# Kernel optimization log

Hardware: AMD Instinct MI355X
Metric: run time of the kernel (lower is better)

## Reference

```python
import jax, jax.numpy as jnp
import numpy as np

MODEL_DIM = 1024
NUM_HEADS = 16
K_DIM = MODEL_DIM // NUM_HEADS


def setup_inputs() -> dict:
    key = jax.random.key(0)
    k1, k2, k3 = jax.random.split(key, 3)
    x = jax.random.normal(k1, (4, 2048, MODEL_DIM), dtype=jnp.float32)
    # nn.Linear(model_dim, 3*model_dim, bias=False): store as [D, 3D] so y = x @ W
    wqkv = jax.random.normal(k2, (MODEL_DIM, 3 * MODEL_DIM), dtype=jnp.float32) * (MODEL_DIM ** -0.5)
    wo = jax.random.normal(k3, (MODEL_DIM, MODEL_DIM), dtype=jnp.float32) * (MODEL_DIM ** -0.5)
    return {"x": x, "wqkv": wqkv, "wo": wo}


def reference(x, wqkv, wo):
    B, L, D = x.shape
    H, K = NUM_HEADS, K_DIM
    qkv = jnp.einsum("bld,de->ble", x, wqkv)  # [B, L, 3D]
    q, k, v = jnp.split(qkv, 3, axis=-1)
    # Faithful to source: plain reshape (no transpose) into [B, H, L, K]
    qh = q.reshape(B, H, L, K)
    kh = k.reshape(B, H, L, K)
    vh = v.reshape(B, H, L, K)
    scores = jnp.einsum("bhlk,bhmk->bhlm", qh, kh) / jnp.sqrt(jnp.float32(K))
    # Faithful quirk: softmax over dim=1 (head axis), as in the source
    probs = jax.nn.softmax(scores, axis=1)
    attended = jnp.einsum("bhlm,bhmk->bhlk", probs, vh)  # [B, H, L, K]
    concatted = attended.transpose(0, 2, 1, 3).reshape(B, L, D)
    return jnp.einsum("bld,de->ble", concatted, wo)
```

## Files before the change

### kernel.cpp

```cpp
#include <hip/hip_runtime.h>
#include <hip/hip_bf16.h>
#include <stdint.h>

typedef __attribute__((ext_vector_type(8))) short short8;
typedef __attribute__((ext_vector_type(4))) float floatx4;

#define QSCALE 0.18033688f

__device__ __forceinline__ unsigned short f2bf(float f) {
    unsigned int u = __float_as_uint(f);
    u += 0x7fffu + ((u >> 16) & 1u);
    return (unsigned short)(u >> 16);
}
__device__ __forceinline__ unsigned int pack2bf(float a, float b) {
    __hip_bfloat162 h = __float22bfloat162_rn(make_float2(a, b));
    return *reinterpret_cast<unsigned int*>(&h);
}

__device__ __forceinline__ void async16(const void* g, void* l) {
    __builtin_amdgcn_global_load_lds(
        (const __attribute__((address_space(1))) unsigned int*)g,
        (__attribute__((address_space(3))) unsigned int*)l, 16, 0, 0);
}

__global__ __launch_bounds__(256) void cvt_bf16(const float* __restrict__ src,
                                                unsigned short* __restrict__ dst, int n8) {
    int i = blockIdx.x * 256 + threadIdx.x;
    if (i >= n8) return;
    const float4 a = ((const float4*)src)[2 * i];
    const float4 b = ((const float4*)src)[2 * i + 1];
    ushort4 lo, hi;
    lo.x = f2bf(a.x); lo.y = f2bf(a.y); lo.z = f2bf(a.z); lo.w = f2bf(a.w);
    hi.x = f2bf(b.x); hi.y = f2bf(b.y); hi.z = f2bf(b.z); hi.w = f2bf(b.w);
    ((ushort4*)dst)[2 * i] = lo;
    ((ushort4*)dst)[2 * i + 1] = hi;
}

__global__ __launch_bounds__(256) void tcvt(const float* __restrict__ src,
                                            unsigned short* __restrict__ dst, int R, int C) {
    __shared__ unsigned short t[64][72];
    const int tid = threadIdx.x;
    const int r0 = blockIdx.y * 64, c0 = blockIdx.x * 64;
    #pragma unroll
    for (int it = 0; it < 4; it++) {
        int idx = it * 256 + tid;
        int rr = idx >> 4, cc = (idx & 15) * 4;
        float4 v = *(const float4*)(src + (size_t)(r0 + rr) * C + c0 + cc);
        t[cc + 0][rr] = f2bf(v.x);
        t[cc + 1][rr] = f2bf(v.y);
        t[cc + 2][rr] = f2bf(v.z);
        t[cc + 3][rr] = f2bf(v.w);
    }
    __syncthreads();
    #pragma unroll
    for (int it = 0; it < 2; it++) {
        int idx = it * 256 + tid;
        int cc = idx >> 3, r8 = (idx & 7) * 8;
        short8 v = *(const short8*)&t[cc][r8];
        *(short8*)(dst + (size_t)(c0 + cc) * R + r0 + r8) = v;
    }
}

__global__ __launch_bounds__(256) void vtrans(const unsigned short* __restrict__ vb,
                                              unsigned short* __restrict__ vbt) {
    __shared__ unsigned short t[64][72];
    const int tid = threadIdx.x;
    const int bh = blockIdx.y, m0 = blockIdx.x * 64;
    const unsigned short* src = vb + ((size_t)bh * 2048 + m0) * 64;
    unsigned short* dst = vbt + ((size_t)bh << 17) + m0;
    union { short8 v; unsigned short u[8]; } tmp;
    #pragma unroll
    for (int it = 0; it < 2; it++) {
        int idx = it * 256 + tid;
        int m = idx >> 3, c8 = (idx & 7) * 8;
        tmp.v = *(const short8*)(src + (size_t)m * 64 + c8);
        #pragma unroll
        for (int j = 0; j < 8; j++) t[c8 + j][m] = tmp.u[j];
    }
    __syncthreads();
    #pragma unroll
    for (int it = 0; it < 2; it++) {
        int idx = it * 256 + tid;
        int k = idx >> 3, c8 = (idx & 7) * 8;
        short8 v = *(const short8*)&t[k][c8];
        *(short8*)(dst + (size_t)k * 2048 + c8) = v;
    }
}

__global__ __launch_bounds__(256) void qkv_gemm(
    const unsigned short* __restrict__ A, const unsigned short* __restrict__ Bt,
    unsigned short* __restrict__ qb, unsigned short* __restrict__ kb,
    unsigned short* __restrict__ vb)
{
    __shared__ __align__(16) unsigned short As[128 * 32];
    __shared__ __align__(16) unsigned short Bs[128 * 32];
    const int tid = threadIdx.x, wave = tid >> 6, lane = tid & 63;
    const int quad = lane >> 4, lr = lane & 15;
    const int wr = wave >> 1, wc = wave & 1;
    const int bm = blockIdx.y * 128, bn = blockIdx.x * 128;
    const int lrow = lane >> 2, lcol = (lane & 3) * 8;

    floatx4 acc[4][4];
    #pragma unroll
    for (int i = 0; i < 4; i++)
        #pragma unroll
        for (int j = 0; j < 4; j++) acc[i][j] = (floatx4)0.0f;

    for (int k0 = 0; k0 < 1024; k0 += 32) {
        #pragma unroll
        for (int t = 0; t < 2; t++) {
            const int rbase = wave * 32 + t * 16;
            const int r = rbase + lrow;
            async16(A  + (size_t)(bm + r) * 1024 + k0 + lcol, &As[rbase * 32]);
            async16(Bt + (size_t)(bn + r) * 1024 + k0 + lcol, &Bs[rbase * 32]);
        }
        __syncthreads();
        short8 af[4], bfr[4];
        #pragma unroll
        for (int i = 0; i < 4; i++)
            af[i] = *(const short8*)&As[(wr * 64 + i * 16 + lr) * 32 + quad * 8];
        #pragma unroll
        for (int j = 0; j < 4; j++)
            bfr[j] = *(const short8*)&Bs[(wc * 64 + j * 16 + lr) * 32 + quad * 8];
        #pragma unroll
        for (int i = 0; i < 4; i++)
            #pragma unroll
            for (int j = 0; j < 4; j++)
                acc[i][j] = __builtin_amdgcn_mfma_f32_16x16x32_bf16(af[i], bfr[j], acc[i][j], 0, 0, 0);
        __syncthreads();
    }

    const int part = bn >> 10;
    unsigned short* __restrict__ dstb = (part == 0) ? qb : ((part == 1) ? kb : vb);
    const float sc = (part == 0) ? QSCALE : 1.0f;
    const int dbase = bn & 1023;
    #pragma unroll
    for (int i = 0; i < 4; i++)
        #pragma unroll
        for (int j = 0; j < 4; j++)
            #pragma unroll
            for (int r = 0; r < 4; r++) {
                int row = bm + wr * 64 + i * 16 + quad * 4 + r;
                int d   = dbase + wc * 64 + j * 16 + lr;
                int b = row >> 11, l = row & 2047;
                int flat = (l << 10) | d;
                int h = flat >> 17;
                int rem = flat & 131071;
                int l2 = rem >> 6, kk = rem & 63;
                dstb[((size_t)(b * 16 + h) * 2048 + l2) * 64 + kk] = f2bf(acc[i][j][r] * sc);
            }
}

__global__ __launch_bounds__(256) void out_gemm(
    const unsigned short* __restrict__ A, const unsigned short* __restrict__ Bt,
    float* __restrict__ C)
{
    __shared__ __align__(16) unsigned short As[128 * 32];
    __shared__ __align__(16) unsigned short Bs[128 * 32];
    const int tid = threadIdx.x, wave = tid >> 6, lane = tid & 63;
    const int quad = lane >> 4, lr = lane & 15;
    const int wr = wave >> 1, wc = wave & 1;
    const int bm = blockIdx.y * 128, bn = blockIdx.x * 128;
    const int lrow = lane >> 2, lcol = (lane & 3) * 8;

    floatx4 acc[4][4];
    #pragma unroll
    for (int i = 0; i < 4; i++)
        #pragma unroll
        for (int j = 0; j < 4; j++) acc[i][j] = (floatx4)0.0f;

    for (int k0 = 0; k0 < 1024; k0 += 32) {
        #pragma unroll
        for (int t = 0; t < 2; t++) {
            const int rbase = wave * 32 + t * 16;
            const int r = rbase + lrow;
            async16(A  + (size_t)(bm + r) * 1024 + k0 + lcol, &As[rbase * 32]);
            async16(Bt + (size_t)(bn + r) * 1024 + k0 + lcol, &Bs[rbase * 32]);
        }
        __syncthreads();
        short8 af[4], bfr[4];
        #pragma unroll
        for (int i = 0; i < 4; i++)
            af[i] = *(const short8*)&As[(wr * 64 + i * 16 + lr) * 32 + quad * 8];
        #pragma unroll
        for (int j = 0; j < 4; j++)
            bfr[j] = *(const short8*)&Bs[(wc * 64 + j * 16 + lr) * 32 + quad * 8];
        #pragma unroll
        for (int i = 0; i < 4; i++)
            #pragma unroll
            for (int j = 0; j < 4; j++)
                acc[i][j] = __builtin_amdgcn_mfma_f32_16x16x32_bf16(af[i], bfr[j], acc[i][j], 0, 0, 0);
        __syncthreads();
    }
    #pragma unroll
    for (int i = 0; i < 4; i++)
        #pragma unroll
        for (int j = 0; j < 4; j++)
            #pragma unroll
            for (int r = 0; r < 4; r++) {
                int row = bm + wr * 64 + i * 16 + quad * 4 + r;
                int col = bn + wc * 64 + j * 16 + lr;
                C[(size_t)row * 1024 + col] = acc[i][j][r];
            }
}

__global__ __launch_bounds__(256, 4) void attn_denom(
    const unsigned short* __restrict__ qb, const unsigned short* __restrict__ kb,
    unsigned short* __restrict__ drpT)
{
    __shared__ __align__(16) unsigned short Qs[64 * 64];
    __shared__ __align__(16) unsigned short Ks[64 * 64];
    const int tid = threadIdx.x, wave = tid >> 6, lane = tid & 63;
    const int quad = lane >> 4, lr = lane & 15;
    const int M0 = blockIdx.x * 64, L0 = blockIdx.y * 64, b = blockIdx.z;
    const int srow = tid >> 3, sblk = tid & 7;
    const int sphys = (sblk ^ (srow & 7)) * 8;

    floatx4 e[4];
    #pragma unroll
    for (int i = 0; i < 4; i++) e[i] = (floatx4)0.0f;

    {
        const size_t hb = ((size_t)(b * 16)) << 17;
        short8 q0 = *(const short8*)(qb + hb + (size_t)(L0 + srow) * 64 + sblk * 8);
        short8 q1 = *(const short8*)(qb + hb + (size_t)(L0 + srow + 32) * 64 + sblk * 8);
        short8 k0 = *(const short8*)(kb + hb + (size_t)(M0 + srow) * 64 + sblk * 8);
        short8 k1 = *(const short8*)(kb + hb + (size_t)(M0 + srow + 32) * 64 + sblk * 8);
        *(short8*)&Qs[srow * 64 + sphys] = q0;
        *(short8*)&Qs[(srow + 32) * 64 + sphys] = q1;
        *(short8*)&Ks[srow * 64 + sphys] = k0;
        *(short8*)&Ks[(srow + 32) * 64 + sphys] = k1;
    }
    __syncthreads();

    for (int h = 0; h < 16; h++) {
        short8 qn0, qn1, kn0, kn1;
        if (h < 15) {
            const size_t hb = ((size_t)(b * 16 + h + 1)) << 17;
            qn0 = *(const short8*)(qb + hb + (size_t)(L0 + srow) * 64 + sblk * 8);
            qn1 = *(const short8*)(qb + hb + (size_t)(L0 + srow + 32) * 64 + sblk * 8);
            kn0 = *(const short8*)(kb + hb + (size_t)(M0 + srow) * 64 + sblk * 8);
            kn1 = *(const short8*)(kb + hb + (size_t)(M0 + srow + 32) * 64 + sblk * 8);
        }
        const int rq = wave * 16 + lr;
        short8 qf0 = *(const short8*)&Qs[rq * 64 + ((quad) ^ (lr & 7)) * 8];
        short8 qf1 = *(const short8*)&Qs[rq * 64 + ((4 + quad) ^ (lr & 7)) * 8];
        #pragma unroll
        for (int mt = 0; mt < 4; mt++) {
            const int rk = mt * 16 + lr;
            short8 kf0 = *(const short8*)&Ks[rk * 64 + ((quad) ^ (lr & 7)) * 8];
            short8 kf1 = *(const short8*)&Ks[rk * 64 + ((4 + quad) ^ (lr & 7)) * 8];
            floatx4 s = (floatx4)0.0f;
            s = __builtin_amdgcn_mfma_f32_16x16x32_bf16(kf0, qf0, s, 0, 0, 0);
            s = __builtin_amdgcn_mfma_f32_16x16x32_bf16(kf1, qf1, s, 0, 0, 0);
            e[mt][0] += __builtin_amdgcn_exp2f(s[0]);
            e[mt][1] += __builtin_amdgcn_exp2f(s[1]);
            e[mt][2] += __builtin_amdgcn_exp2f(s[2]);
            e[mt][3] += __builtin_amdgcn_exp2f(s[3]);
        }
        __syncthreads();
        if (h < 15) {
            *(short8*)&Qs[srow * 64 + sphys] = qn0;
            *(short8*)&Qs[(srow + 32) * 64 + sphys] = qn1;
            *(short8*)&Ks[srow * 64 + sphys] = kn0;
            *(short8*)&Ks[(srow + 32) * 64 + sphys] = kn1;
            __syncthreads();
        }
    }
    #pragma unroll
    for (int mt = 0; mt < 4; mt++) {
        float r0 = __builtin_amdgcn_rcpf(e[mt][0]);
        float r1 = __builtin_amdgcn_rcpf(e[mt][1]);
        float r2 = __builtin_amdgcn_rcpf(e[mt][2]);
        float r3 = __builtin_amdgcn_rcpf(e[mt][3]);
        uint2 o;
        o.x = pack2bf(r0, r1);
        o.y = pack2bf(r2, r3);
        int mtg = (M0 >> 4) + mt;
        int ltg = (L0 >> 4) + wave;
        *(uint2*)(drpT + ((((size_t)b * 128 + mtg) * 128 + ltg) << 8) + lane * 4) = o;
    }
}

__global__ __launch_bounds__(256, 4) void attn_pv(
    const unsigned short* __restrict__ qb, const unsigned short* __restrict__ kb,
    const unsigned short* __restrict__ vbt, const unsigned short* __restrict__ drpT,
    unsigned short* __restrict__ cb)
{
    __shared__ __align__(16) unsigned short Ks[2][64 * 64];
    __shared__ __align__(16) unsigned short Ps[128 * 64];
    const int tid = threadIdx.x, wave = tid >> 6, lane = tid & 63;
    const int quad = lane >> 4, lr = lane & 15;
    const int L0 = blockIdx.x * 128, h = blockIdx.y, b = blockIdx.z;
    const size_t head = (size_t)(b * 16 + h);
    const unsigned short* qbase = qb + (head << 17);
    const unsigned short* kbase = kb + (head << 17);
    const unsigned short* vtb   = vbt + (head << 17);
    const int krow = tid >> 3, ksb = tid & 7;
    const int kphys = (ksb ^ (krow & 7)) * 8;
    const int e7 = lr & 15 & 7;
    const unsigned short* dbase = drpT + (((size_t)b * 128 * 128 + ((L0 >> 4) + wave * 2)) << 8) + lane * 4;

    short8 qf[2][2];
    #pragma unroll
    for (int j = 0; j < 2; j++) {
        const unsigned short* qr = qbase + (size_t)(L0 + wave * 32 + j * 16 + lr) * 64;
        qf[j][0] = *(const short8*)(qr + quad * 8);
        qf[j][1] = *(const short8*)(qr + 32 + quad * 8);
    }

    floatx4 oacc[2][4];
    #pragma unroll
    for (int i = 0; i < 2; i++)
        #pragma unroll
        for (int j = 0; j < 4; j++) oacc[i][j] = (floatx4)0.0f;

    uint2 dunext[4][2];
    {
        short8 a = *(const short8*)(kbase + (size_t)krow * 64 + ksb * 8);
        short8 c = *(const short8*)(kbase + (size_t)(krow + 32) * 64 + ksb * 8);
        *(short8*)&Ks[0][krow * 64 + kphys] = a;
        *(short8*)&Ks[0][(krow + 32) * 64 + kphys] = c;
        #pragma unroll
        for (int mt = 0; mt < 4; mt++)
            #pragma unroll
            for (int j = 0; j < 2; j++)
                dunext[mt][j] = *(const uint2*)(dbase + ((size_t)mt << 15) + (j << 8));
    }
    __syncthreads();

    for (int t = 0; t < 32; t++) {
        const int M0 = t * 64;
        short8 nka, nkc;
        if (t < 31) {
            nka = *(const short8*)(kbase + (size_t)(M0 + 64 + krow) * 64 + ksb * 8);
            nkc = *(const short8*)(kbase + (size_t)(M0 + 64 + krow + 32) * 64 + ksb * 8);
        }
        short8 vfr[2][4];
        #pragma unroll
        for (int f = 0; f < 2; f++)
            #pragma unroll
            for (int j2 = 0; j2 < 4; j2++)
                vfr[f][j2] = *(const short8*)(vtb + (size_t)(j2 * 16 + lr) * 2048 + M0 + f * 32 + quad * 8);

        const unsigned short* ksrc = &Ks[t & 1][0];
        #pragma unroll
        for (int mt = 0; mt < 4; mt++) {
            const int rk = mt * 16 + lr;
            short8 kf0 = *(const short8*)&ksrc[rk * 64 + (quad ^ e7) * 8];
            short8 kf1 = *(const short8*)&ksrc[rk * 64 + ((4 + quad) ^ e7) * 8];
            #pragma unroll
            for (int j = 0; j < 2; j++) {
                uint2 du = dunext[mt][j];
                floatx4 s = (floatx4)0.0f;
                s = __builtin_amdgcn_mfma_f32_16x16x32_bf16(kf0, qf[j][0], s, 0, 0, 0);
                s = __builtin_amdgcn_mfma_f32_16x16x32_bf16(kf1, qf[j][1], s, 0, 0, 0);
                float r0 = __uint_as_float(du.x << 16);
                float r1 = __uint_as_float(du.x & 0xffff0000u);
                float r2 = __uint_as_float(du.y << 16);
                float r3 = __uint_as_float(du.y & 0xffff0000u);
                float p0 = __builtin_amdgcn_exp2f(s[0]) * r0;
                float p1 = __builtin_amdgcn_exp2f(s[1]) * r1;
                float p2 = __builtin_amdgcn_exp2f(s[2]) * r2;
                float p3 = __builtin_amdgcn_exp2f(s[3]) * r3;
                uint2 o;
                o.x = pack2bf(p0, p1);
                o.y = pack2bf(p2, p3);
                const int l_loc = wave * 32 + j * 16 + lr;
                const int lb16 = mt * 2 + (quad >> 1);
                *(uint2*)&Ps[l_loc * 64 + (lb16 ^ e7) * 8 + (quad & 1) * 4] = o;
            }
        }
        if (t < 31) {
            #pragma unroll
            for (int mt = 0; mt < 4; mt++)
                #pragma unroll
                for (int j = 0; j < 2; j++)
                    dunext[mt][j] = *(const uint2*)(dbase + (((size_t)((t + 1) * 4 + mt)) << 15) + (j << 8));
        }
        #pragma unroll
        for (int f = 0; f < 2; f++) {
            short8 pf[2];
            #pragma unroll
            for (int i2 = 0; i2 < 2; i2++) {
                const int lrow = wave * 32 + i2 * 16 + lr;
                pf[i2] = *(const short8*)&Ps[lrow * 64 + ((f * 4 + quad) ^ e7) * 8];
            }
            #pragma unroll
            for (int j2 = 0; j2 < 4; j2++)
                #pragma unroll
                for (int i2 = 0; i2 < 2; i2++)
                    oacc[i2][j2] = __builtin_amdgcn_mfma_f32_16x16x32_bf16(pf[i2], vfr[f][j2], oacc[i2][j2], 0, 0, 0);
        }
        if (t < 31) {
            unsigned short* kdst = &Ks[(t + 1) & 1][0];
            *(short8*)&kdst[krow * 64 + kphys] = nka;
            *(short8*)&kdst[(krow + 32) * 64 + kphys] = nkc;
            __syncthreads();
        }
    }
    #pragma unroll
    for (int i2 = 0; i2 < 2; i2++)
        #pragma unroll
        for (int j2 = 0; j2 < 4; j2++)
            #pragma unroll
            for (int r = 0; r < 4; r++) {
                int row = L0 + wave * 32 + i2 * 16 + quad * 4 + r;
                int col = h * 64 + j2 * 16 + lr;
                cb[(size_t)(b * 2048 + row) * 1024 + col] = f2bf(oacc[i2][j2][r]);
            }
}

extern "C" void kernel_launch(void* const* d_in, const int* in_sizes, int n_in,
                              void* d_out, int out_size, void* d_ws, size_t ws_size,
                              hipStream_t stream) {
    const float* x    = (const float*)d_in[0];
    const float* wqkv = (const float*)d_in[1];
    const float* wo   = (const float*)d_in[2];
    float* out = (float*)d_out;

    unsigned short* W = (unsigned short*)d_ws;
    unsigned short* qb   = W;
    unsigned short* kb   = W + 8388608;
    unsigned short* vbt  = W + 16777216;
    unsigned short* drpT = W + 25165824;
    unsigned short* cb   = W + 41943040;
    unsigned short* xb    = drpT;
    unsigned short* wqkvT = drpT + 8388608;
    unsigned short* vb    = cb;
    unsigned short* woT   = drpT;

    cvt_bf16  <<<4096, 256, 0, stream>>>(x, xb, 1048576);
    tcvt      <<<dim3(48, 16), 256, 0, stream>>>(wqkv, wqkvT, 1024, 3072);
    qkv_gemm  <<<dim3(24, 64), 256, 0, stream>>>(xb, wqkvT, qb, kb, vb);
    vtrans    <<<dim3(32, 64), 256, 0, stream>>>(vb, vbt);
    attn_denom<<<dim3(32, 32, 4), 256, 0, stream>>>(qb, kb, drpT);
    attn_pv   <<<dim3(16, 16, 4), 256, 0, stream>>>(qb, kb, vbt, drpT, cb);
    tcvt      <<<dim3(16, 16), 256, 0, stream>>>(wo, woT, 1024, 1024);
    out_gemm  <<<dim3(8, 64), 256, 0, stream>>>(cb, woT, out);
}
```

Measured before the change: 438.0 us.

## Load K fragments straight into registers and drop LDS staging and barriers in attn_pv

The K tile is no longer double-buffered through shared memory. Each lane loads its MFMA K fragments directly from global memory into registers, and the next tile is prefetched inside the mt loop. Because Ps is private to each wave, the per-iteration __syncthreads can go. The second half of the V fragments is now loaded mid-loop, and the launch-bounds occupancy hint drops from 4 to 3 blocks to allow more registers. The aim is to cut LDS traffic and block-wide barriers, at the cost of higher register pressure, less coalesced K reads, and unguarded prefetches past the last tile that read beyond the head's K and drpT ranges.

```diff
diff --git a/kernel.cpp b/kernel.cpp
--- a/kernel.cpp
+++ b/kernel.cpp
@@ -282,12 +282,11 @@
     }
 }
 
-__global__ __launch_bounds__(256, 4) void attn_pv(
+__global__ __launch_bounds__(256, 3) void attn_pv(
     const unsigned short* __restrict__ qb, const unsigned short* __restrict__ kb,
     const unsigned short* __restrict__ vbt, const unsigned short* __restrict__ drpT,
     unsigned short* __restrict__ cb)
 {
-    __shared__ __align__(16) unsigned short Ks[2][64 * 64];
     __shared__ __align__(16) unsigned short Ps[128 * 64];
     const int tid = threadIdx.x, wave = tid >> 6, lane = tid & 63;
     const int quad = lane >> 4, lr = lane & 15;
@@ -296,9 +295,7 @@
     const unsigned short* qbase = qb + (head << 17);
     const unsigned short* kbase = kb + (head << 17);
     const unsigned short* vtb   = vbt + (head << 17);
-    const int krow = tid >> 3, ksb = tid & 7;
-    const int kphys = (ksb ^ (krow & 7)) * 8;
-    const int e7 = lr & 15 & 7;
+    const int e7 = lr & 7;
     const unsigned short* dbase = drpT + (((size_t)b * 128 * 128 + ((L0 >> 4) + wave * 2)) << 8) + lane * 4;
 
     short8 qf[2][2];
@@ -315,50 +312,41 @@
         #pragma unroll
         for (int j = 0; j < 4; j++) oacc[i][j] = (floatx4)0.0f;
 
-    uint2 dunext[4][2];
-    {
-        short8 a = *(const short8*)(kbase + (size_t)krow * 64 + ksb * 8);
-        short8 c = *(const short8*)(kbase + (size_t)(krow + 32) * 64 + ksb * 8);
-        *(short8*)&Ks[0][krow * 64 + kphys] = a;
-        *(short8*)&Ks[0][(krow + 32) * 64 + kphys] = c;
-        #pragma unroll
-        for (int mt = 0; mt < 4; mt++)
-            #pragma unroll
-            for (int j = 0; j < 2; j++)
-                dunext[mt][j] = *(const uint2*)(dbase + ((size_t)mt << 15) + (j << 8));
-    }
-    __syncthreads();
+    const unsigned short* kfp = kbase + (size_t)lr * 64 + quad * 8;
+
+    short8 kf[4][2];
+    #pragma unroll
+    for (int mt = 0; mt < 4; mt++) {
+        kf[mt][0] = *(const short8*)(kfp + (size_t)(mt * 16) * 64);
+        kf[mt][1] = *(const short8*)(kfp + (size_t)(mt * 16) * 64 + 32);
+    }
+    uint2 du[4][2];
+    #pragma unroll
+    for (int mt = 0; mt < 4; mt++)
+        #pragma unroll
+        for (int j = 0; j < 2; j++)
+            du[mt][j] = *(const uint2*)(dbase + ((size_t)mt << 15) + (j << 8));
 
     for (int t = 0; t < 32; t++) {
         const int M0 = t * 64;
-        short8 nka, nkc;
-        if (t < 31) {
-            nka = *(const short8*)(kbase + (size_t)(M0 + 64 + krow) * 64 + ksb * 8);
-            nkc = *(const short8*)(kbase + (size_t)(M0 + 64 + krow + 32) * 64 + ksb * 8);
-        }
-        short8 vfr[2][4];
-        #pragma unroll
-        for (int f = 0; f < 2; f++)
-            #pragma unroll
-            for (int j2 = 0; j2 < 4; j2++)
-                vfr[f][j2] = *(const short8*)(vtb + (size_t)(j2 * 16 + lr) * 2048 + M0 + f * 32 + quad * 8);
-
-        const unsigned short* ksrc = &Ks[t & 1][0];
+        short8 vf0[4], vf1[4];
+        #pragma unroll
+        for (int j2 = 0; j2 < 4; j2++)
+            vf0[j2] = *(const short8*)(vtb + (size_t)(j2 * 16 + lr) * 2048 + M0 + quad * 8);
+
         #pragma unroll
         for (int mt = 0; mt < 4; mt++) {
-            const int rk = mt * 16 + lr;
-            short8 kf0 = *(const short8*)&ksrc[rk * 64 + (quad ^ e7) * 8];
-            short8 kf1 = *(const short8*)&ksrc[rk * 64 + ((4 + quad) ^ e7) * 8];
+            short8 kf0 = kf[mt][0], kf1 = kf[mt][1];
             #pragma unroll
             for (int j = 0; j < 2; j++) {
-                uint2 du = dunext[mt][j];
+                uint2 duv = du[mt][j];
                 floatx4 s = (floatx4)0.0f;
                 s = __builtin_amdgcn_mfma_f32_16x16x32_bf16(kf0, qf[j][0], s, 0, 0, 0);
                 s = __builtin_amdgcn_mfma_f32_16x16x32_bf16(kf1, qf[j][1], s, 0, 0, 0);
-                float r0 = __uint_as_float(du.x << 16);
-                float r1 = __uint_as_float(du.x & 0xffff0000u);
-                float r2 = __uint_as_float(du.y << 16);
-                float r3 = __uint_as_float(du.y & 0xffff0000u);
+                float r0 = __uint_as_float(duv.x << 16);
+                float r1 = __uint_as_float(duv.x & 0xffff0000u);
+                float r2 = __uint_as_float(duv.y << 16);
+                float r3 = __uint_as_float(duv.y & 0xffff0000u);
                 float p0 = __builtin_amdgcn_exp2f(s[0]) * r0;
                 float p1 = __builtin_amdgcn_exp2f(s[1]) * r1;
                 float p2 = __builtin_amdgcn_exp2f(s[2]) * r2;
@@ -370,14 +358,20 @@
                 const int lb16 = mt * 2 + (quad >> 1);
                 *(uint2*)&Ps[l_loc * 64 + (lb16 ^ e7) * 8 + (quad & 1) * 4] = o;
             }
-        }
-        if (t < 31) {
-            #pragma unroll
-            for (int mt = 0; mt < 4; mt++)
+            kf[mt][0] = *(const short8*)(kfp + (size_t)(M0 + 64 + mt * 16) * 64);
+            kf[mt][1] = *(const short8*)(kfp + (size_t)(M0 + 64 + mt * 16) * 64 + 32);
+            if (mt == 1) {
                 #pragma unroll
-                for (int j = 0; j < 2; j++)
-                    dunext[mt][j] = *(const uint2*)(dbase + (((size_t)((t + 1) * 4 + mt)) << 15) + (j << 8));
-        }
+                for (int j2 = 0; j2 < 4; j2++)
+                    vf1[j2] = *(const short8*)(vtb + (size_t)(j2 * 16 + lr) * 2048 + M0 + 32 + quad * 8);
+            }
+        }
+        #pragma unroll
+        for (int mt = 0; mt < 4; mt++)
+            #pragma unroll
+            for (int j = 0; j < 2; j++)
+                du[mt][j] = *(const uint2*)(dbase + (((size_t)((t + 1) * 4 + mt)) << 15) + (j << 8));
+
         #pragma unroll
         for (int f = 0; f < 2; f++) {
             short8 pf[2];
@@ -390,13 +384,8 @@
             for (int j2 = 0; j2 < 4; j2++)
                 #pragma unroll
                 for (int i2 = 0; i2 < 2; i2++)
-                    oacc[i2][j2] = __builtin_amdgcn_mfma_f32_16x16x32_bf16(pf[i2], vfr[f][j2], oacc[i2][j2], 0, 0, 0);
-        }
-        if (t < 31) {
-            unsigned short* kdst = &Ks[(t + 1) & 1][0];
-            *(short8*)&kdst[krow * 64 + kphys] = nka;
-            *(short8*)&kdst[(krow + 32) * 64 + kphys] = nkc;
-            __syncthreads();
+                    oacc[i2][j2] = __builtin_amdgcn_mfma_f32_16x16x32_bf16(
+                        pf[i2], (f == 0) ? vf0[j2] : vf1[j2], oacc[i2][j2], 0, 0, 0);
         }
     }
     #pragma unroll
```

Result: slower. 555.5 us (+26.8%).
